# Optimization experiments

Measured on AMD Instinct MI355X. Metric: run time of the kernel, lower is better.

Reference implementation:

```python
import jax, jax.numpy as jnp
import numpy as np

N_NODES = 100000
N_EDGES = 1600000
N_GRAPHS = 512
HIDDEN = 128
N_LAYERS = 3


def setup_inputs() -> dict:
    key = jax.random.key(0)
    ks = jax.random.split(key, 16)
    X = jax.random.normal(ks[0], (N_NODES, HIDDEN), dtype=jnp.float32)
    edge_index = jax.random.randint(ks[1], (2, N_EDGES), 0, N_NODES, dtype=jnp.int64)
    batch = jnp.sort(jax.random.randint(ks[2], (N_NODES,), 0, N_GRAPHS, dtype=jnp.int64))
    s = 1.0 / np.sqrt(HIDDEN)
    mlp_w1 = jax.random.normal(ks[3], (N_LAYERS, HIDDEN, HIDDEN), dtype=jnp.float32) * s
    mlp_b1 = jnp.zeros((N_LAYERS, HIDDEN), dtype=jnp.float32)
    mlp_w2 = jax.random.normal(ks[4], (N_LAYERS, HIDDEN, HIDDEN), dtype=jnp.float32) * s
    mlp_b2 = jnp.zeros((N_LAYERS, HIDDEN), dtype=jnp.float32)
    cls_w1 = jax.random.normal(ks[5], (HIDDEN * N_LAYERS, HIDDEN), dtype=jnp.float32) / np.sqrt(HIDDEN * N_LAYERS)
    cls_b1 = jnp.zeros((HIDDEN,), dtype=jnp.float32)
    cls_w2 = jax.random.normal(ks[6], (HIDDEN, HIDDEN), dtype=jnp.float32) * s
    cls_b2 = jnp.zeros((HIDDEN,), dtype=jnp.float32)
    cls_w3 = jax.random.normal(ks[7], (HIDDEN, 1), dtype=jnp.float32) * s
    cls_b3 = jnp.zeros((1,), dtype=jnp.float32)
    return {"X": X, "edge_index": edge_index, "batch": batch,
            "mlp_w1": mlp_w1, "mlp_b1": mlp_b1, "mlp_w2": mlp_w2, "mlp_b2": mlp_b2,
            "cls_w1": cls_w1, "cls_b1": cls_b1, "cls_w2": cls_w2, "cls_b2": cls_b2,
            "cls_w3": cls_w3, "cls_b3": cls_b3}


def reference(X, edge_index, batch, mlp_w1, mlp_b1, mlp_w2, mlp_b2,
              cls_w1, cls_b1, cls_w2, cls_b2, cls_w3, cls_b3):
    src, dst = edge_index[0], edge_index[1]
    xs = []
    for l in range(N_LAYERS):
        # GIN aggregation: sum_{j in N(i)} x_j ; eps = 0 so add self feature
        agg = jax.ops.segment_sum(X[src], dst, num_segments=N_NODES)  # [N, H]
        z = X + agg
        # 2-layer MLP update
        h = jax.nn.relu(z @ mlp_w1[l] + mlp_b1[l])
        h = h @ mlp_w2[l] + mlp_b2[l]
        # dropout is identity in eval; then relu
        X = jax.nn.relu(h)
        # global sum pooling per graph
        xs.append(jax.ops.segment_sum(X, batch, num_segments=N_GRAPHS))  # [G, H]
    h = jnp.concatenate(xs, axis=-1)  # JK 'cat' -> [G, H*L]
    h = jax.nn.relu(h @ cls_w1 + cls_b1)
    h = jax.nn.relu(h @ cls_w2 + cls_b2)
    logits = h @ cls_w3 + cls_b3  # [G, 1]
    return logits
```

## Files before the change

kernel.cpp:

```cpp
#include <hip/hip_runtime.h>
#include <hip/hip_fp16.h>
#include <cstddef>
#include <cstdint>

#define N_NODES   100000
#define N_EDGES   1600000
#define N_GRAPHS  512
#define HIDDEN    128
#define N_LAYERS  3

#define N_WIN        400
#define WIN_NODES    (N_NODES / N_WIN)
#define PLACE_BLOCKS 128
#define PCHUNK       (N_EDGES / PLACE_BLOCKS)

#define F2H_BLOCKS   ((N_NODES * HIDDEN / 8) / 256)
#define WCONV_BLOCKS (N_LAYERS * 2 * 16)
#define GB_BLOCKS    2
#define PREPC_BLOCKS (PLACE_BLOCKS + F2H_BLOCKS + WCONV_BLOCKS + GB_BLOCKS)

typedef _Float16 half8  __attribute__((ext_vector_type(8)));
typedef _Float16 half4v __attribute__((ext_vector_type(4)));
typedef _Float16 half2v __attribute__((ext_vector_type(2)));
typedef float    float8 __attribute__((ext_vector_type(8)));
typedef float    floatx4 __attribute__((ext_vector_type(4)));
typedef float    floatx2 __attribute__((ext_vector_type(2)));

__global__ __launch_bounds__(256) void prep_count_kernel(const float* __restrict__ X,
                                                         unsigned char* __restrict__ outq,
                                                         const float* __restrict__ w1,
                                                         const float* __restrict__ w2,
                                                         __half* __restrict__ wt1,
                                                         __half* __restrict__ wt2,
                                                         const int* __restrict__ batch,
                                                         int* __restrict__ gstart,
                                                         const int* __restrict__ dst,
                                                         int* __restrict__ counts) {
    __shared__ float tile[32][33];
    __shared__ int   cs[N_WIN];
    const int b = blockIdx.x;
    if (b < PLACE_BLOCKS) {
        for (int i = threadIdx.x; i < N_WIN; i += 256) cs[i] = 0;
        __syncthreads();
        const int4* d4 = (const int4*)(dst + b * PCHUNK);
        for (int i = threadIdx.x; i < PCHUNK / 4; i += 256) {
            int4 d = d4[i];
            atomicAdd(&cs[d.x / WIN_NODES], 1);
            atomicAdd(&cs[d.y / WIN_NODES], 1);
            atomicAdd(&cs[d.z / WIN_NODES], 1);
            atomicAdd(&cs[d.w / WIN_NODES], 1);
        }
        __syncthreads();
        for (int i = threadIdx.x; i < N_WIN; i += 256)
            counts[i * PLACE_BLOCKS + b] = cs[i];
    } else if (b < PLACE_BLOCKS + F2H_BLOCKS) {
        int t = (b - PLACE_BLOCKS) * 256 + threadIdx.x;
        const float4* in4 = (const float4*)X;
        float4 a = in4[t * 2 + 0];
        float4 c = in4[t * 2 + 1];
        unsigned r0 = 0, r1 = 0;
        r0 = __builtin_amdgcn_cvt_pk_fp8_f32(a.x, a.y, r0, false);
        r0 = __builtin_amdgcn_cvt_pk_fp8_f32(a.z, a.w, r0, true);
        r1 = __builtin_amdgcn_cvt_pk_fp8_f32(c.x, c.y, r1, false);
        r1 = __builtin_amdgcn_cvt_pk_fp8_f32(c.z, c.w, r1, true);
        ((uint2*)outq)[t] = make_uint2(r0, r1);
    } else if (b < PLACE_BLOCKS + F2H_BLOCKS + WCONV_BLOCKS) {
        const int bb = b - PLACE_BLOCKS - F2H_BLOCKS;
        const int mat = bb & 1;
        const int tt = (bb >> 1) & 15;
        const int l  = bb >> 5;
        const int ti = (tt >> 2) * 32, tj = (tt & 3) * 32;
        const float* W = (mat ? w2 : w1) + (size_t)l * HIDDEN * HIDDEN;
        __half* WT = (mat ? wt2 : wt1) + (size_t)l * HIDDEN * HIDDEN;
        const int r = threadIdx.x >> 5;
        const int c = threadIdx.x & 31;
#pragma unroll
        for (int rr = 0; rr < 4; ++rr)
            tile[r + 8 * rr][c] = W[(size_t)(ti + r + 8 * rr) * HIDDEN + tj + c];
        __syncthreads();
#pragma unroll
        for (int rr = 0; rr < 4; ++rr)
            WT[(size_t)(tj + r + 8 * rr) * HIDDEN + ti + c] =
                __float2half(tile[c][r + 8 * rr]);
    } else {
        const int g = (b - PLACE_BLOCKS - F2H_BLOCKS - WCONV_BLOCKS) * 256 + threadIdx.x;
        if (g < N_GRAPHS) {
            int lo = 0, hi = N_NODES;
            while (lo < hi) {
                int mid = (lo + hi) >> 1;
                if (batch[mid] < g) lo = mid + 1; else hi = mid;
            }
            gstart[g] = lo;
        }
        if (g == 0) gstart[N_GRAPHS] = N_NODES;
    }
}

__global__ __launch_bounds__(512) void win_place_kernel(const int* __restrict__ src,
                                                        const int* __restrict__ dst,
                                                        const int* __restrict__ counts,
                                                        int* __restrict__ colsum,
                                                        int2* __restrict__ wedge) {
    __shared__ int ws[512];
    __shared__ int off[N_WIN];
    const int t = threadIdx.x;
    const int b = blockIdx.x;

    int total = 0, part = 0;
    if (t < N_WIN) {
        const int* col = counts + t * PLACE_BLOCKS;
#pragma unroll 4
        for (int bb = 0; bb < PLACE_BLOCKS; ++bb) {
            int v = col[bb];
            total += v;
            if (bb < b) part += v;
        }
        if (b == 0) colsum[t] = total;
    }
    ws[t] = (t < N_WIN) ? total : 0;
    __syncthreads();
#pragma unroll
    for (int o = 1; o < 512; o <<= 1) {
        int u = (t >= o) ? ws[t - o] : 0;
        __syncthreads();
        ws[t] += u;
        __syncthreads();
    }
    if (t < N_WIN) off[t] = part + ((t == 0) ? 0 : ws[t - 1]);
    __syncthreads();
    const int4* d4 = (const int4*)(dst + b * PCHUNK);
    const int4* s4 = (const int4*)(src + b * PCHUNK);
    for (int i = t; i < PCHUNK / 4; i += 512) {
        int4 d = d4[i];
        int4 s = s4[i];
        int p0 = atomicAdd(&off[d.x / WIN_NODES], 1); wedge[p0] = make_int2(d.x, s.x);
        int p1 = atomicAdd(&off[d.y / WIN_NODES], 1); wedge[p1] = make_int2(d.y, s.y);
        int p2 = atomicAdd(&off[d.z / WIN_NODES], 1); wedge[p2] = make_int2(d.z, s.z);
        int p3 = atomicAdd(&off[d.w / WIN_NODES], 1); wedge[p3] = make_int2(d.w, s.w);
    }
}

__global__ __launch_bounds__(512) void win_csr_kernel(const int2* __restrict__ wedge,
                                                      const int* __restrict__ colsum,
                                                      int* __restrict__ row_ptr,
                                                      int* __restrict__ csr_src) {
    __shared__ int ws[512];
    __shared__ int cnt[WIN_NODES];
    __shared__ int bb[2];
    const int w = blockIdx.x, n0 = w * WIN_NODES, t = threadIdx.x;
    ws[t] = (t < N_WIN) ? colsum[t] : 0;
    __syncthreads();
#pragma unroll
    for (int o = 1; o < 512; o <<= 1) {
        int u = (t >= o) ? ws[t - o] : 0;
        __syncthreads();
        ws[t] += u;
        __syncthreads();
    }
    if (t == 0) { bb[0] = (w > 0) ? ws[w - 1] : 0; bb[1] = ws[w]; }
    if (w == N_WIN - 1 && t == 0) row_ptr[N_NODES] = ws[N_WIN - 1];
    for (int i = t; i < WIN_NODES; i += 512) cnt[i] = 0;
    __syncthreads();
    const int b0 = bb[0], b1 = bb[1];
    for (int e = b0 + t; e < b1; e += 512)
        atomicAdd(&cnt[wedge[e].x - n0], 1);
    __syncthreads();
    ws[t] = (t < WIN_NODES) ? cnt[t] : 0;
    __syncthreads();
#pragma unroll
    for (int o = 1; o < 512; o <<= 1) {
        int u = (t >= o) ? ws[t - o] : 0;
        __syncthreads();
        ws[t] += u;
        __syncthreads();
    }
    const int excl = (t == 0) ? 0 : ws[t - 1];
    if (t < WIN_NODES) {
        row_ptr[n0 + t] = b0 + excl;
        cnt[t] = b0 + excl;
    }
    __syncthreads();
    for (int e = b0 + t; e < b1; e += 512) {
        int2 ed = wedge[e];
        int p = atomicAdd(&cnt[ed.x - n0], 1);
        csr_src[p] = ed.y;
    }
}

__device__ __forceinline__ void acc_fp8x16(floatx2* acc, uint4 v) {
    acc[0] += __builtin_amdgcn_cvt_pk_f32_fp8(v.x, false);
    acc[1] += __builtin_amdgcn_cvt_pk_f32_fp8(v.x, true);
    acc[2] += __builtin_amdgcn_cvt_pk_f32_fp8(v.y, false);
    acc[3] += __builtin_amdgcn_cvt_pk_f32_fp8(v.y, true);
    acc[4] += __builtin_amdgcn_cvt_pk_f32_fp8(v.z, false);
    acc[5] += __builtin_amdgcn_cvt_pk_f32_fp8(v.z, true);
    acc[6] += __builtin_amdgcn_cvt_pk_f32_fp8(v.w, false);
    acc[7] += __builtin_amdgcn_cvt_pk_f32_fp8(v.w, true);
}

__device__ __forceinline__ void gather_body(int wave, int lane,
                                            const unsigned char* __restrict__ Xq,
                                            __half* __restrict__ Zh,
                                            const int* __restrict__ row_ptr,
                                            const int* __restrict__ csr_src) {
    const int grp = lane >> 3;
    const int m   = lane & 7;
    const uint4* Q = (const uint4*)Xq;

    floatx2 acc[8];
#pragma unroll
    for (int j = 0; j < 8; ++j) acc[j] = floatx2{0.f, 0.f};

    if (grp == 0) {
        uint4 v = Q[(size_t)wave * 8 + m];
        acc_fp8x16(acc, v);
    }

    int k = row_ptr[wave];
    const int end = row_ptr[wave + 1];

    for (; k + 16 <= end; k += 16) {
        int n0 = csr_src[k + grp];
        int n1 = csr_src[k + 8 + grp];
        uint4 v0 = Q[(size_t)n0 * 8 + m];
        uint4 v1 = Q[(size_t)n1 * 8 + m];
        acc_fp8x16(acc, v0);
        acc_fp8x16(acc, v1);
    }
    if (k + 8 <= end) {
        int n0 = csr_src[k + grp];
        uint4 v0 = Q[(size_t)n0 * 8 + m];
        acc_fp8x16(acc, v0);
        k += 8;
    }
    int rem = end - k;
    if (grp < rem) {
        int n0 = csr_src[k + grp];
        uint4 v0 = Q[(size_t)n0 * 8 + m];
        acc_fp8x16(acc, v0);
    }

    half2v hh[8];
#pragma unroll
    for (int j = 0; j < 8; ++j) {
        hh[j][0] = (_Float16)acc[j][0];
        hh[j][1] = (_Float16)acc[j][1];
    }
#pragma unroll
    for (int j = 0; j < 8; ++j) {
        int b = __shfl_xor(__builtin_bit_cast(int, hh[j]), 8);
        hh[j] = hh[j] + __builtin_bit_cast(half2v, b);
    }
#pragma unroll
    for (int j = 0; j < 8; ++j) {
        int b = __shfl_xor(__builtin_bit_cast(int, hh[j]), 16);
        hh[j] = hh[j] + __builtin_bit_cast(half2v, b);
    }
#pragma unroll
    for (int j = 0; j < 8; ++j) {
        int b = __shfl_xor(__builtin_bit_cast(int, hh[j]), 32);
        hh[j] = hh[j] + __builtin_bit_cast(half2v, b);
    }

    if (grp == 0) {
        half8 o0, o1;
#pragma unroll
        for (int j = 0; j < 4; ++j) {
            o0[2 * j] = hh[j][0]; o0[2 * j + 1] = hh[j][1];
        }
#pragma unroll
        for (int j = 0; j < 4; ++j) {
            o1[2 * j] = hh[4 + j][0]; o1[2 * j + 1] = hh[4 + j][1];
        }
        ((half8*)(Zh + (size_t)wave * HIDDEN + 16 * m))[0] = o0;
        ((half8*)(Zh + (size_t)wave * HIDDEN + 16 * m))[1] = o1;
    }
}

__global__ void gather_kernel(const unsigned char* __restrict__ Xq,
                              __half* __restrict__ Zh,
                              const int* __restrict__ row_ptr,
                              const int* __restrict__ csr_src) {
    int wave = (blockIdx.x * blockDim.x + threadIdx.x) >> 6;
    if (wave >= N_NODES) return;
    gather_body(wave, threadIdx.x & 63, Xq, Zh, row_ptr, csr_src);
}

__device__ __forceinline__ void gpool_body(int g,
                                           const __half* __restrict__ Hpool,
                                           const int* __restrict__ gstart,
                                           float* __restrict__ pooled, int layer) {
    __shared__ float red[16][16][8];
    const int f8 = threadIdx.x & 15;
    const int qt = threadIdx.x >> 4;
    const int s = gstart[g], e = gstart[g + 1];

    float acc[8];
#pragma unroll
    for (int j = 0; j < 8; ++j) acc[j] = 0.f;

    for (int n = s + qt; n < e; n += 16) {
        half8 v = ((const half8*)(Hpool + (size_t)n * HIDDEN))[f8];
#pragma unroll
        for (int j = 0; j < 8; ++j) acc[j] += (float)v[j];
    }
#pragma unroll
    for (int j = 0; j < 8; ++j) red[qt][f8][j] = acc[j];
    __syncthreads();

    if (threadIdx.x < 128) {
        const int c = threadIdx.x;
        float sum = 0.f;
#pragma unroll
        for (int p = 0; p < 16; ++p) sum += red[p][c >> 3][c & 7];
        pooled[(size_t)g * (HIDDEN * N_LAYERS) + layer * HIDDEN + c] = sum;
    }
}

#define POOL_BLKS N_GRAPHS
__global__ __launch_bounds__(256) void gather_pool_kernel(const unsigned char* __restrict__ Xq,
                                                          const __half* __restrict__ Hpool,
                                                          __half* __restrict__ Zh,
                                                          const int* __restrict__ row_ptr,
                                                          const int* __restrict__ csr_src,
                                                          const int* __restrict__ gstart,
                                                          float* __restrict__ pooled,
                                                          int prev_layer) {
    if (blockIdx.x < POOL_BLKS) {
        gpool_body(blockIdx.x, Hpool, gstart, pooled, prev_layer);
        return;
    }
    int wave = ((blockIdx.x - POOL_BLKS) * 256 + threadIdx.x) >> 6;
    if (wave >= N_NODES) return;
    gather_body(wave, threadIdx.x & 63, Xq, Zh, row_ptr, csr_src);
}

__global__ __launch_bounds__(256) void gpool_cls_kernel(const __half* __restrict__ Xh,
                                                        const int* __restrict__ gstart,
                                                        const float* __restrict__ pooled,
                                                        const float* __restrict__ w1,
                                                        const float* __restrict__ b1,
                                                        const float* __restrict__ w2,
                                                        const float* __restrict__ b2,
                                                        const float* __restrict__ w3,
                                                        const float* __restrict__ b3,
                                                        float* __restrict__ out) {
    __shared__ float red[16][16][8];
    __shared__ float hin[HIDDEN * N_LAYERS];
    __shared__ float h1v[HIDDEN];
    __shared__ float redc[HIDDEN];
    const int g   = blockIdx.x;
    const int tid = threadIdx.x;
    const int f8  = tid & 15;
    const int qt  = tid >> 4;
    const int s = gstart[g], e = gstart[g + 1];

    for (int i = tid; i < 2 * HIDDEN; i += 256)
        hin[i] = pooled[(size_t)g * (HIDDEN * N_LAYERS) + i];

    float acc[8];
#pragma unroll
    for (int j = 0; j < 8; ++j) acc[j] = 0.f;
    for (int n = s + qt; n < e; n += 16) {
        half8 v = ((const half8*)(Xh + (size_t)n * HIDDEN))[f8];
#pragma unroll
        for (int j = 0; j < 8; ++j) acc[j] += (float)v[j];
    }
#pragma unroll
    for (int j = 0; j < 8; ++j) red[qt][f8][j] = acc[j];
    __syncthreads();
    if (tid < 128) {
        float sum = 0.f;
#pragma unroll
        for (int p = 0; p < 16; ++p) sum += red[p][tid >> 3][tid & 7];
        hin[2 * HIDDEN + tid] = sum;
    }
    __syncthreads();

    if (tid < 128) {
        float sacc = 0.f;
        for (int k = 0; k < HIDDEN * N_LAYERS; ++k)
            sacc += hin[k] * w1[(size_t)k * HIDDEN + tid];
        h1v[tid] = fmaxf(sacc + b1[tid], 0.f);
    }
    __syncthreads();
    if (tid < 128) {
        float s2 = 0.f;
        for (int k = 0; k < HIDDEN; ++k) s2 += h1v[k] * w2[(size_t)k * HIDDEN + tid];
        s2 = fmaxf(s2 + b2[tid], 0.f);
        redc[tid] = s2 * w3[tid];
    }
    __syncthreads();
    for (int off = 64; off > 0; off >>= 1) {
        if (tid < off) redc[tid] += redc[tid + off];
        __syncthreads();
    }
    if (tid == 0) out[g] = redc[0] + b3[0];
}

#define MMF_BLOCKS 512
__global__ __launch_bounds__(512, 4) void mlp_ws_kernel(const __half* __restrict__ A,
                                                        const __half* __restrict__ Wt1,
                                                        const __half* __restrict__ Wt2,
                                                        const float* __restrict__ b1,
                                                        const float* __restrict__ b2,
                                                        __half* __restrict__ C16,
                                                        unsigned char* __restrict__ Q8) {
    __shared__ _Float16 hs[2][16][128];

    const int tid  = threadIdx.x;
    const int wv   = tid >> 6;
    const int lane = tid & 63;
    const int m    = lane & 15;
    const int q    = lane >> 4;
    const int NTILES = N_NODES / 16;

    half8 wf1[4], wf2[4];
    float bl1[4], bl2[4];
    {
        const half8* W1row = (const half8*)(Wt1 + (size_t)(wv * 16 + m) * HIDDEN);
        const half8* W2row = (const half8*)(Wt2 + (size_t)(wv * 16 + m) * HIDDEN);
#pragma unroll
        for (int c = 0; c < 4; ++c) { wf1[c] = W1row[c * 4 + q]; wf2[c] = W2row[c * 4 + q]; }
#pragma unroll
        for (int r = 0; r < 4; ++r) {
            bl1[r] = b1[wv * 16 + q * 4 + r];
            bl2[r] = b2[wv * 16 + q * 4 + r];
        }
    }

    _Float16* hwr0 = &hs[0][m][(((2 * wv + (q >> 1)) ^ m) << 3) + ((q & 1) << 2)];
    _Float16* hwr1 = &hs[1][m][(((2 * wv + (q >> 1)) ^ m) << 3) + ((q & 1) << 2)];
    const _Float16* hrd0 = &hs[0][m][0];
    const _Float16* hrd1 = &hs[1][m][0];

    int t = blockIdx.x;
    half8 c0, c1, c2, c3, p0, p1, p2, p3;
    {
        const half8* Ar = (const half8*)(A + (size_t)(t * 16 + m) * HIDDEN);
        c0 = Ar[q]; c1 = Ar[4 + q]; c2 = Ar[8 + q]; c3 = Ar[12 + q];
    }
    if (t + MMF_BLOCKS < NTILES) {
        const half8* Ar = (const half8*)(A + (size_t)((t + MMF_BLOCKS) * 16 + m) * HIDDEN);
        p0 = Ar[q]; p1 = Ar[4 + q]; p2 = Ar[8 + q]; p3 = Ar[12 + q];
    }

    int buf = 0;
    while (true) {
        const int t2 = t + 2 * MMF_BLOCKS;
        half8 f0, f1, f2, f3;
        if (t2 < NTILES) {
            const half8* Ar = (const half8*)(A + (size_t)(t2 * 16 + m) * HIDDEN);
            f0 = Ar[q]; f1 = Ar[4 + q]; f2 = Ar[8 + q]; f3 = Ar[12 + q];
        }

        {
            floatx4 acc = {0.f, 0.f, 0.f, 0.f};
            acc = __builtin_amdgcn_mfma_f32_16x16x32_f16(wf1[0], c0, acc, 0, 0, 0);
            acc = __builtin_amdgcn_mfma_f32_16x16x32_f16(wf1[1], c1, acc, 0, 0, 0);
            acc = __builtin_amdgcn_mfma_f32_16x16x32_f16(wf1[2], c2, acc, 0, 0, 0);
            acc = __builtin_amdgcn_mfma_f32_16x16x32_f16(wf1[3], c3, acc, 0, 0, 0);
            half4v o;
#pragma unroll
            for (int r = 0; r < 4; ++r) o[r] = (_Float16)fmaxf(acc[r] + bl1[r], 0.f);
            *(half4v*)(buf ? hwr1 : hwr0) = o;
        }
        __builtin_amdgcn_sched_barrier(0);
        asm volatile("s_waitcnt lgkmcnt(0)" ::: "memory");
        __builtin_amdgcn_s_barrier();
        __builtin_amdgcn_sched_barrier(0);

        {
            const _Float16* hr = buf ? hrd1 : hrd0;
            half8 h0 = *(const half8*)(hr + (((0 + q) ^ m) << 3));
            half8 h1 = *(const half8*)(hr + (((4 + q) ^ m) << 3));
            half8 h2 = *(const half8*)(hr + (((8 + q) ^ m) << 3));
            half8 h3 = *(const half8*)(hr + (((12 + q) ^ m) << 3));
            floatx4 acc = {0.f, 0.f, 0.f, 0.f};
            acc = __builtin_amdgcn_mfma_f32_16x16x32_f16(wf2[0], h0, acc, 0, 0, 0);
            acc = __builtin_amdgcn_mfma_f32_16x16x32_f16(wf2[1], h1, acc, 0, 0, 0);
            acc = __builtin_amdgcn_mfma_f32_16x16x32_f16(wf2[2], h2, acc, 0, 0, 0);
            acc = __builtin_amdgcn_mfma_f32_16x16x32_f16(wf2[3], h3, acc, 0, 0, 0);
            float v0 = fmaxf(acc[0] + bl2[0], 0.f);
            float v1 = fmaxf(acc[1] + bl2[1], 0.f);
            float v2 = fmaxf(acc[2] + bl2[2], 0.f);
            float v3 = fmaxf(acc[3] + bl2[3], 0.f);
            const size_t base = (size_t)(t * 16 + m) * HIDDEN + wv * 16 + q * 4;
            half4v o;
            o[0] = (_Float16)v0; o[1] = (_Float16)v1;
            o[2] = (_Float16)v2; o[3] = (_Float16)v3;
            *(half4v*)(C16 + base) = o;
            if (Q8) {
                unsigned r0 = 0;
                r0 = __builtin_amdgcn_cvt_pk_fp8_f32(v0, v1, r0, false);
                r0 = __builtin_amdgcn_cvt_pk_fp8_f32(v2, v3, r0, true);
                *(unsigned*)(Q8 + base) = r0;
            }
        }

        if (t + MMF_BLOCKS >= NTILES) break;
        t += MMF_BLOCKS;
        c0 = p0; c1 = p1; c2 = p2; c3 = p3;
        p0 = f0; p1 = f1; p2 = f2; p3 = f3;
        buf ^= 1;
    }
}

extern "C" void kernel_launch(void* const* d_in, const int* in_sizes, int n_in,
                              void* d_out, int out_size, void* d_ws, size_t ws_size,
                              hipStream_t stream) {
    const float* X     = (const float*)d_in[0];
    const int*   ei    = (const int*)d_in[1];
    const int*   batch = (const int*)d_in[2];
    const float* w1all = (const float*)d_in[3];
    const float* b1all = (const float*)d_in[4];
    const float* w2all = (const float*)d_in[5];
    const float* b2all = (const float*)d_in[6];
    const float* cw1   = (const float*)d_in[7];
    const float* cb1   = (const float*)d_in[8];
    const float* cw2   = (const float*)d_in[9];
    const float* cb2   = (const float*)d_in[10];
    const float* cw3   = (const float*)d_in[11];
    const float* cb3   = (const float*)d_in[12];
    float* out = (float*)d_out;

    const int* src = ei;
    const int* dst = ei + N_EDGES;

    char* p = (char*)d_ws;
    auto alloc2 = [&](size_t bytes) {
        char* r = p;
        p += (bytes + 255) & ~(size_t)255;
        return r;
    };
    __half* hA      = (__half*)alloc2((size_t)N_NODES * HIDDEN * sizeof(__half));
    __half* hB      = (__half*)alloc2((size_t)N_NODES * HIDDEN * sizeof(__half));
    __half* zh      = (__half*)alloc2((size_t)N_NODES * HIDDEN * sizeof(__half));
    unsigned char* qbuf = (unsigned char*)alloc2((size_t)N_NODES * HIDDEN);
    __half* wt1     = (__half*)alloc2((size_t)N_LAYERS * HIDDEN * HIDDEN * sizeof(__half));
    __half* wt2     = (__half*)alloc2((size_t)N_LAYERS * HIDDEN * HIDDEN * sizeof(__half));
    int2*   wedge   = (int2*)alloc2((size_t)N_EDGES * sizeof(int2));
    int*    csr     = (int*)alloc2((size_t)N_EDGES * sizeof(int));
    int*    rowp    = (int*)alloc2((size_t)(N_NODES + 1) * sizeof(int));
    int*    counts  = (int*)alloc2((size_t)PLACE_BLOCKS * N_WIN * sizeof(int));
    int*    colsum  = (int*)alloc2((size_t)N_WIN * sizeof(int));
    int*    gstart  = (int*)alloc2((size_t)(N_GRAPHS + 1) * sizeof(int));
    float*  pooled  = (float*)alloc2((size_t)N_GRAPHS * HIDDEN * N_LAYERS * sizeof(float));

    prep_count_kernel<<<PREPC_BLOCKS, 256, 0, stream>>>(X, qbuf, w1all, w2all,
                                                        wt1, wt2, batch, gstart,
                                                        dst, counts);
    win_place_kernel<<<PLACE_BLOCKS, 512, 0, stream>>>(src, dst, counts, colsum, wedge);
    win_csr_kernel<<<N_WIN, 512, 0, stream>>>(wedge, colsum, rowp, csr);

    const int gat_grid = (N_NODES + 3) / 4;

    __half* hcur = nullptr;
    for (int l = 0; l < N_LAYERS; ++l) {
        __half* hnext = (l & 1) ? hA : hB;
        const bool emit = (l < N_LAYERS - 1);
        if (l == 0) {
            gather_kernel<<<gat_grid, 256, 0, stream>>>(qbuf, zh, rowp, csr);
        } else {
            gather_pool_kernel<<<gat_grid + POOL_BLKS, 256, 0, stream>>>(
                qbuf, hcur, zh, rowp, csr, gstart, pooled, l - 1);
        }
        mlp_ws_kernel<<<MMF_BLOCKS, 512, 0, stream>>>(zh,
                                                      wt1 + (size_t)l * HIDDEN * HIDDEN,
                                                      wt2 + (size_t)l * HIDDEN * HIDDEN,
                                                      b1all + (size_t)l * HIDDEN,
                                                      b2all + (size_t)l * HIDDEN,
                                                      hnext,
                                                      emit ? qbuf : (unsigned char*)nullptr);
        hcur = hnext;
    }

    gpool_cls_kernel<<<N_GRAPHS, 256, 0, stream>>>(hcur, gstart, pooled,
                                                   cw1, cb1, cw2, cb2, cw3, cb3, out);
}
```

Measured before the change: 426.9 us.

## Fuse neighbor gather into MLP kernel via LDS-staged tiles

Merges the per-node fp8 neighbor aggregation and the two-layer MFMA MLP into one persistent kernel. Each wave gathers two node rows into a swizzled LDS tile, which then feeds the MFMA directly. This removes the fp16 Z buffer write and read and one launch per layer. The fp8 feature buffer is now ping-ponged, since the kernel reads the previous features while writing new ones. The cost is that the gather latency is no longer hidden by the old register prefetch pipeline, and each tile now has an extra barrier.

```diff
diff --git a/kernel.cpp b/kernel.cpp
--- a/kernel.cpp
+++ b/kernel.cpp
@@ -22,7 +22,6 @@
 typedef _Float16 half8  __attribute__((ext_vector_type(8)));
 typedef _Float16 half4v __attribute__((ext_vector_type(4)));
 typedef _Float16 half2v __attribute__((ext_vector_type(2)));
-typedef float    float8 __attribute__((ext_vector_type(8)));
 typedef float    floatx4 __attribute__((ext_vector_type(4)));
 typedef float    floatx2 __attribute__((ext_vector_type(2)));
 
@@ -198,13 +197,13 @@
     acc[7] += __builtin_amdgcn_cvt_pk_f32_fp8(v.w, true);
 }
 
-__device__ __forceinline__ void gather_body(int wave, int lane,
-                                            const unsigned char* __restrict__ Xq,
-                                            __half* __restrict__ Zh,
-                                            const int* __restrict__ row_ptr,
-                                            const int* __restrict__ csr_src) {
+__device__ __forceinline__ void gather_node_lds(int node, int lane,
+                                                const unsigned char* __restrict__ Xq,
+                                                const int* __restrict__ row_ptr,
+                                                const int* __restrict__ csr_src,
+                                                _Float16* __restrict__ ztrow, int row) {
     const int grp = lane >> 3;
-    const int m   = lane & 7;
+    const int gm  = lane & 7;
     const uint4* Q = (const uint4*)Xq;
 
     floatx2 acc[8];
@@ -212,31 +211,31 @@
     for (int j = 0; j < 8; ++j) acc[j] = floatx2{0.f, 0.f};
 
     if (grp == 0) {
-        uint4 v = Q[(size_t)wave * 8 + m];
+        uint4 v = Q[(size_t)node * 8 + gm];
         acc_fp8x16(acc, v);
     }
 
-    int k = row_ptr[wave];
-    const int end = row_ptr[wave + 1];
+    int k = row_ptr[node];
+    const int end = row_ptr[node + 1];
 
     for (; k + 16 <= end; k += 16) {
         int n0 = csr_src[k + grp];
         int n1 = csr_src[k + 8 + grp];
-        uint4 v0 = Q[(size_t)n0 * 8 + m];
-        uint4 v1 = Q[(size_t)n1 * 8 + m];
+        uint4 v0 = Q[(size_t)n0 * 8 + gm];
+        uint4 v1 = Q[(size_t)n1 * 8 + gm];
         acc_fp8x16(acc, v0);
         acc_fp8x16(acc, v1);
     }
     if (k + 8 <= end) {
         int n0 = csr_src[k + grp];
-        uint4 v0 = Q[(size_t)n0 * 8 + m];
+        uint4 v0 = Q[(size_t)n0 * 8 + gm];
         acc_fp8x16(acc, v0);
         k += 8;
     }
     int rem = end - k;
     if (grp < rem) {
         int n0 = csr_src[k + grp];
-        uint4 v0 = Q[(size_t)n0 * 8 + m];
+        uint4 v0 = Q[(size_t)n0 * 8 + gm];
         acc_fp8x16(acc, v0);
     }
 
@@ -265,32 +264,19 @@
     if (grp == 0) {
         half8 o0, o1;
 #pragma unroll
-        for (int j = 0; j < 4; ++j) {
-            o0[2 * j] = hh[j][0]; o0[2 * j + 1] = hh[j][1];
-        }
-#pragma unroll
-        for (int j = 0; j < 4; ++j) {
-            o1[2 * j] = hh[4 + j][0]; o1[2 * j + 1] = hh[4 + j][1];
-        }
-        ((half8*)(Zh + (size_t)wave * HIDDEN + 16 * m))[0] = o0;
-        ((half8*)(Zh + (size_t)wave * HIDDEN + 16 * m))[1] = o1;
-    }
-}
-
-__global__ void gather_kernel(const unsigned char* __restrict__ Xq,
-                              __half* __restrict__ Zh,
-                              const int* __restrict__ row_ptr,
-                              const int* __restrict__ csr_src) {
-    int wave = (blockIdx.x * blockDim.x + threadIdx.x) >> 6;
-    if (wave >= N_NODES) return;
-    gather_body(wave, threadIdx.x & 63, Xq, Zh, row_ptr, csr_src);
-}
-
-__device__ __forceinline__ void gpool_body(int g,
-                                           const __half* __restrict__ Hpool,
-                                           const int* __restrict__ gstart,
-                                           float* __restrict__ pooled, int layer) {
-    __shared__ float red[16][16][8];
+        for (int j = 0; j < 4; ++j) { o0[2 * j] = hh[j][0]; o0[2 * j + 1] = hh[j][1]; }
+#pragma unroll
+        for (int j = 0; j < 4; ++j) { o1[2 * j] = hh[4 + j][0]; o1[2 * j + 1] = hh[4 + j][1]; }
+        *(half8*)&ztrow[((2 * gm) ^ row) << 3]     = o0;
+        *(half8*)&ztrow[((2 * gm + 1) ^ row) << 3] = o1;
+    }
+}
+
+__device__ __forceinline__ void gpool_body512(int g,
+                                              const __half* __restrict__ H,
+                                              const int* __restrict__ gstart,
+                                              float* __restrict__ pooled, int layer) {
+    __shared__ float red[32][16][8];
     const int f8 = threadIdx.x & 15;
     const int qt = threadIdx.x >> 4;
     const int s = gstart[g], e = gstart[g + 1];
@@ -298,115 +284,48 @@
     float acc[8];
 #pragma unroll
     for (int j = 0; j < 8; ++j) acc[j] = 0.f;
-
-    for (int n = s + qt; n < e; n += 16) {
-        half8 v = ((const half8*)(Hpool + (size_t)n * HIDDEN))[f8];
+    for (int n = s + qt; n < e; n += 32) {
+        half8 v = ((const half8*)(H + (size_t)n * HIDDEN))[f8];
 #pragma unroll
         for (int j = 0; j < 8; ++j) acc[j] += (float)v[j];
     }
 #pragma unroll
     for (int j = 0; j < 8; ++j) red[qt][f8][j] = acc[j];
     __syncthreads();
-
     if (threadIdx.x < 128) {
         const int c = threadIdx.x;
         float sum = 0.f;
 #pragma unroll
-        for (int p = 0; p < 16; ++p) sum += red[p][c >> 3][c & 7];
+        for (int p = 0; p < 32; ++p) sum += red[p][c >> 3][c & 7];
         pooled[(size_t)g * (HIDDEN * N_LAYERS) + layer * HIDDEN + c] = sum;
     }
 }
 
 #define POOL_BLKS N_GRAPHS
-__global__ __launch_bounds__(256) void gather_pool_kernel(const unsigned char* __restrict__ Xq,
-                                                          const __half* __restrict__ Hpool,
-                                                          __half* __restrict__ Zh,
-                                                          const int* __restrict__ row_ptr,
-                                                          const int* __restrict__ csr_src,
-                                                          const int* __restrict__ gstart,
-                                                          float* __restrict__ pooled,
-                                                          int prev_layer) {
-    if (blockIdx.x < POOL_BLKS) {
-        gpool_body(blockIdx.x, Hpool, gstart, pooled, prev_layer);
+#define GM_BLOCKS 1024
+__global__ __launch_bounds__(512, 4) void gather_mlp_kernel(
+        const unsigned char* __restrict__ Xq,
+        const __half* __restrict__ Hpool,
+        const int* __restrict__ row_ptr,
+        const int* __restrict__ csr_src,
+        const __half* __restrict__ Wt1,
+        const __half* __restrict__ Wt2,
+        const float* __restrict__ b1,
+        const float* __restrict__ b2,
+        const int* __restrict__ gstart,
+        float* __restrict__ pooled,
+        int prev_layer,
+        __half* __restrict__ C16,
+        unsigned char* __restrict__ Q8) {
+    __shared__ _Float16 zt[2][16][128];
+    __shared__ _Float16 hs[2][16][128];
+
+    const bool has_pool = (prev_layer >= 0);
+    if (has_pool && blockIdx.x < POOL_BLKS) {
+        gpool_body512(blockIdx.x, Hpool, gstart, pooled, prev_layer);
         return;
     }
-    int wave = ((blockIdx.x - POOL_BLKS) * 256 + threadIdx.x) >> 6;
-    if (wave >= N_NODES) return;
-    gather_body(wave, threadIdx.x & 63, Xq, Zh, row_ptr, csr_src);
-}
-
-__global__ __launch_bounds__(256) void gpool_cls_kernel(const __half* __restrict__ Xh,
-                                                        const int* __restrict__ gstart,
-                                                        const float* __restrict__ pooled,
-                                                        const float* __restrict__ w1,
-                                                        const float* __restrict__ b1,
-                                                        const float* __restrict__ w2,
-                                                        const float* __restrict__ b2,
-                                                        const float* __restrict__ w3,
-                                                        const float* __restrict__ b3,
-                                                        float* __restrict__ out) {
-    __shared__ float red[16][16][8];
-    __shared__ float hin[HIDDEN * N_LAYERS];
-    __shared__ float h1v[HIDDEN];
-    __shared__ float redc[HIDDEN];
-    const int g   = blockIdx.x;
-    const int tid = threadIdx.x;
-    const int f8  = tid & 15;
-    const int qt  = tid >> 4;
-    const int s = gstart[g], e = gstart[g + 1];
-
-    for (int i = tid; i < 2 * HIDDEN; i += 256)
-        hin[i] = pooled[(size_t)g * (HIDDEN * N_LAYERS) + i];
-
-    float acc[8];
-#pragma unroll
-    for (int j = 0; j < 8; ++j) acc[j] = 0.f;
-    for (int n = s + qt; n < e; n += 16) {
-        half8 v = ((const half8*)(Xh + (size_t)n * HIDDEN))[f8];
-#pragma unroll
-        for (int j = 0; j < 8; ++j) acc[j] += (float)v[j];
-    }
-#pragma unroll
-    for (int j = 0; j < 8; ++j) red[qt][f8][j] = acc[j];
-    __syncthreads();
-    if (tid < 128) {
-        float sum = 0.f;
-#pragma unroll
-        for (int p = 0; p < 16; ++p) sum += red[p][tid >> 3][tid & 7];
-        hin[2 * HIDDEN + tid] = sum;
-    }
-    __syncthreads();
-
-    if (tid < 128) {
-        float sacc = 0.f;
-        for (int k = 0; k < HIDDEN * N_LAYERS; ++k)
-            sacc += hin[k] * w1[(size_t)k * HIDDEN + tid];
-        h1v[tid] = fmaxf(sacc + b1[tid], 0.f);
-    }
-    __syncthreads();
-    if (tid < 128) {
-        float s2 = 0.f;
-        for (int k = 0; k < HIDDEN; ++k) s2 += h1v[k] * w2[(size_t)k * HIDDEN + tid];
-        s2 = fmaxf(s2 + b2[tid], 0.f);
-        redc[tid] = s2 * w3[tid];
-    }
-    __syncthreads();
-    for (int off = 64; off > 0; off >>= 1) {
-        if (tid < off) redc[tid] += redc[tid + off];
-        __syncthreads();
-    }
-    if (tid == 0) out[g] = redc[0] + b3[0];
-}
-
-#define MMF_BLOCKS 512
-__global__ __launch_bounds__(512, 4) void mlp_ws_kernel(const __half* __restrict__ A,
-                                                        const __half* __restrict__ Wt1,
-                                                        const __half* __restrict__ Wt2,
-                                                        const float* __restrict__ b1,
-                                                        const float* __restrict__ b2,
-                                                        __half* __restrict__ C16,
-                                                        unsigned char* __restrict__ Q8) {
-    __shared__ _Float16 hs[2][16][128];
+    const int gb = blockIdx.x - (has_pool ? POOL_BLKS : 0);
 
     const int tid  = threadIdx.x;
     const int wv   = tid >> 6;
@@ -429,41 +348,13 @@
         }
     }
 
-    _Float16* hwr0 = &hs[0][m][(((2 * wv + (q >> 1)) ^ m) << 3) + ((q & 1) << 2)];
-    _Float16* hwr1 = &hs[1][m][(((2 * wv + (q >> 1)) ^ m) << 3) + ((q & 1) << 2)];
-    const _Float16* hrd0 = &hs[0][m][0];
-    const _Float16* hrd1 = &hs[1][m][0];
-
-    int t = blockIdx.x;
-    half8 c0, c1, c2, c3, p0, p1, p2, p3;
-    {
-        const half8* Ar = (const half8*)(A + (size_t)(t * 16 + m) * HIDDEN);
-        c0 = Ar[q]; c1 = Ar[4 + q]; c2 = Ar[8 + q]; c3 = Ar[12 + q];
-    }
-    if (t + MMF_BLOCKS < NTILES) {
-        const half8* Ar = (const half8*)(A + (size_t)((t + MMF_BLOCKS) * 16 + m) * HIDDEN);
-        p0 = Ar[q]; p1 = Ar[4 + q]; p2 = Ar[8 + q]; p3 = Ar[12 + q];
-    }
-
     int buf = 0;
-    while (true) {
-        const int t2 = t + 2 * MMF_BLOCKS;
-        half8 f0, f1, f2, f3;
-        if (t2 < NTILES) {
-            const half8* Ar = (const half8*)(A + (size_t)(t2 * 16 + m) * HIDDEN);
-            f0 = Ar[q]; f1 = Ar[4 + q]; f2 = Ar[8 + q]; f3 = Ar[12 + q];
-        }
-
-        {
-            floatx4 acc = {0.f, 0.f, 0.f, 0.f};
-            acc = __builtin_amdgcn_mfma_f32_16x16x32_f16(wf1[0], c0, acc, 0, 0, 0);
-            acc = __builtin_amdgcn_mfma_f32_16x16x32_f16(wf1[1], c1, acc, 0, 0, 0);
-            acc = __builtin_amdgcn_mfma_f32_16x16x32_f16(wf1[2], c2, acc, 0, 0, 0);
-            acc = __builtin_amdgcn_mfma_f32_16x16x32_f16(wf1[3], c3, acc, 0, 0, 0);
-            half4v o;
-#pragma unroll
-            for (int r = 0; r < 4; ++r) o[r] = (_Float16)fmaxf(acc[r] + bl1[r], 0.f);
-            *(half4v*)(buf ? hwr1 : hwr0) = o;
+    for (int t = gb; t < NTILES; t += GM_BLOCKS) {
+#pragma unroll
+        for (int s = 0; s < 2; ++s) {
+            const int row = 2 * wv + s;
+            gather_node_lds(t * 16 + row, lane, Xq, row_ptr, csr_src,
+                            &zt[buf][row][0], row);
         }
         __builtin_amdgcn_sched_barrier(0);
         asm volatile("s_waitcnt lgkmcnt(0)" ::: "memory");
@@ -471,7 +362,28 @@
         __builtin_amdgcn_sched_barrier(0);
 
         {
-            const _Float16* hr = buf ? hrd1 : hrd0;
+            const _Float16* ar = &zt[buf][m][0];
+            half8 a0 = *(const half8*)(ar + (((0 + q) ^ m) << 3));
+            half8 a1 = *(const half8*)(ar + (((4 + q) ^ m) << 3));
+            half8 a2 = *(const half8*)(ar + (((8 + q) ^ m) << 3));
+            half8 a3 = *(const half8*)(ar + (((12 + q) ^ m) << 3));
+            floatx4 acc = {0.f, 0.f, 0.f, 0.f};
+            acc = __builtin_amdgcn_mfma_f32_16x16x32_f16(wf1[0], a0, acc, 0, 0, 0);
+            acc = __builtin_amdgcn_mfma_f32_16x16x32_f16(wf1[1], a1, acc, 0, 0, 0);
+            acc = __builtin_amdgcn_mfma_f32_16x16x32_f16(wf1[2], a2, acc, 0, 0, 0);
+            acc = __builtin_amdgcn_mfma_f32_16x16x32_f16(wf1[3], a3, acc, 0, 0, 0);
+            half4v o;
+#pragma unroll
+            for (int r = 0; r < 4; ++r) o[r] = (_Float16)fmaxf(acc[r] + bl1[r], 0.f);
+            *(half4v*)&hs[buf][m][(((2 * wv + (q >> 1)) ^ m) << 3) + ((q & 1) << 2)] = o;
+        }
+        __builtin_amdgcn_sched_barrier(0);
+        asm volatile("s_waitcnt lgkmcnt(0)" ::: "memory");
+        __builtin_amdgcn_s_barrier();
+        __builtin_amdgcn_sched_barrier(0);
+
+        {
+            const _Float16* hr = &hs[buf][m][0];
             half8 h0 = *(const half8*)(hr + (((0 + q) ^ m) << 3));
             half8 h1 = *(const half8*)(hr + (((4 + q) ^ m) << 3));
             half8 h2 = *(const half8*)(hr + (((8 + q) ^ m) << 3));
@@ -497,13 +409,71 @@
                 *(unsigned*)(Q8 + base) = r0;
             }
         }
-
-        if (t + MMF_BLOCKS >= NTILES) break;
-        t += MMF_BLOCKS;
-        c0 = p0; c1 = p1; c2 = p2; c3 = p3;
-        p0 = f0; p1 = f1; p2 = f2; p3 = f3;
         buf ^= 1;
     }
+}
+
+__global__ __launch_bounds__(256) void gpool_cls_kernel(const __half* __restrict__ Xh,
+                                                        const int* __restrict__ gstart,
+                                                        const float* __restrict__ pooled,
+                                                        const float* __restrict__ w1,
+                                                        const float* __restrict__ b1,
+                                                        const float* __restrict__ w2,
+                                                        const float* __restrict__ b2,
+                                                        const float* __restrict__ w3,
+                                                        const float* __restrict__ b3,
+                                                        float* __restrict__ out) {
+    __shared__ float red[16][16][8];
+    __shared__ float hin[HIDDEN * N_LAYERS];
+    __shared__ float h1v[HIDDEN];
+    __shared__ float redc[HIDDEN];
+    const int g   = blockIdx.x;
+    const int tid = threadIdx.x;
+    const int f8  = tid & 15;
+    const int qt  = tid >> 4;
+    const int s = gstart[g], e = gstart[g + 1];
+
+    for (int i = tid; i < 2 * HIDDEN; i += 256)
+        hin[i] = pooled[(size_t)g * (HIDDEN * N_LAYERS) + i];
+
+    float acc[8];
+#pragma unroll
+    for (int j = 0; j < 8; ++j) acc[j] = 0.f;
+    for (int n = s + qt; n < e; n += 16) {
+        half8 v = ((const half8*)(Xh + (size_t)n * HIDDEN))[f8];
+#pragma unroll
+        for (int j = 0; j < 8; ++j) acc[j] += (float)v[j];
+    }
+#pragma unroll
+    for (int j = 0; j < 8; ++j) red[qt][f8][j] = acc[j];
+    __syncthreads();
+    if (tid < 128) {
+        float sum = 0.f;
+#pragma unroll
+        for (int p = 0; p < 16; ++p) sum += red[p][tid >> 3][tid & 7];
+        hin[2 * HIDDEN + tid] = sum;
+    }
+    __syncthreads();
+
+    if (tid < 128) {
+        float sacc = 0.f;
+        for (int k = 0; k < HIDDEN * N_LAYERS; ++k)
+            sacc += hin[k] * w1[(size_t)k * HIDDEN + tid];
+        h1v[tid] = fmaxf(sacc + b1[tid], 0.f);
+    }
+    __syncthreads();
+    if (tid < 128) {
+        float s2 = 0.f;
+        for (int k = 0; k < HIDDEN; ++k) s2 += h1v[k] * w2[(size_t)k * HIDDEN + tid];
+        s2 = fmaxf(s2 + b2[tid], 0.f);
+        redc[tid] = s2 * w3[tid];
+    }
+    __syncthreads();
+    for (int off = 64; off > 0; off >>= 1) {
+        if (tid < off) redc[tid] += redc[tid + off];
+        __syncthreads();
+    }
+    if (tid == 0) out[g] = redc[0] + b3[0];
 }
 
 extern "C" void kernel_launch(void* const* d_in, const int* in_sizes, int n_in,
@@ -535,8 +505,8 @@
     };
     __half* hA      = (__half*)alloc2((size_t)N_NODES * HIDDEN * sizeof(__half));
     __half* hB      = (__half*)alloc2((size_t)N_NODES * HIDDEN * sizeof(__half));
-    __half* zh      = (__half*)alloc2((size_t)N_NODES * HIDDEN * sizeof(__half));
-    unsigned char* qbuf = (unsigned char*)alloc2((size_t)N_NODES * HIDDEN);
+    unsigned char* qA = (unsigned char*)alloc2((size_t)N_NODES * HIDDEN);
+    unsigned char* qB = (unsigned char*)alloc2((size_t)N_NODES * HIDDEN);
     __half* wt1     = (__half*)alloc2((size_t)N_LAYERS * HIDDEN * HIDDEN * sizeof(__half));
     __half* wt2     = (__half*)alloc2((size_t)N_LAYERS * HIDDEN * HIDDEN * sizeof(__half));
     int2*   wedge   = (int2*)alloc2((size_t)N_EDGES * sizeof(int2));
@@ -547,32 +517,29 @@
     int*    gstart  = (int*)alloc2((size_t)(N_GRAPHS + 1) * sizeof(int));
     float*  pooled  = (float*)alloc2((size_t)N_GRAPHS * HIDDEN * N_LAYERS * sizeof(float));
 
-    prep_count_kernel<<<PREPC_BLOCKS, 256, 0, stream>>>(X, qbuf, w1all, w2all,
+    prep_count_kernel<<<PREPC_BLOCKS, 256, 0, stream>>>(X, qA, w1all, w2all,
                                                         wt1, wt2, batch, gstart,
                                                         dst, counts);
     win_place_kernel<<<PLACE_BLOCKS, 512, 0, stream>>>(src, dst, counts, colsum, wedge);
     win_csr_kernel<<<N_WIN, 512, 0, stream>>>(wedge, colsum, rowp, csr);
 
-    const int gat_grid = (N_NODES + 3) / 4;
-
+    unsigned char* qin  = qA;
+    unsigned char* qout = qB;
     __half* hcur = nullptr;
     for (int l = 0; l < N_LAYERS; ++l) {
         __half* hnext = (l & 1) ? hA : hB;
         const bool emit = (l < N_LAYERS - 1);
-        if (l == 0) {
-            gather_kernel<<<gat_grid, 256, 0, stream>>>(qbuf, zh, rowp, csr);
-        } else {
-            gather_pool_kernel<<<gat_grid + POOL_BLKS, 256, 0, stream>>>(
-                qbuf, hcur, zh, rowp, csr, gstart, pooled, l - 1);
-        }
-        mlp_ws_kernel<<<MMF_BLOCKS, 512, 0, stream>>>(zh,
-                                                      wt1 + (size_t)l * HIDDEN * HIDDEN,
-                                                      wt2 + (size_t)l * HIDDEN * HIDDEN,
-                                                      b1all + (size_t)l * HIDDEN,
-                                                      b2all + (size_t)l * HIDDEN,
-                                                      hnext,
-                                                      emit ? qbuf : (unsigned char*)nullptr);
+        const int grid = GM_BLOCKS + ((l > 0) ? POOL_BLKS : 0);
+        gather_mlp_kernel<<<grid, 512, 0, stream>>>(
+            qin, hcur, rowp, csr,
+            wt1 + (size_t)l * HIDDEN * HIDDEN,
+            wt2 + (size_t)l * HIDDEN * HIDDEN,
+            b1all + (size_t)l * HIDDEN,
+            b2all + (size_t)l * HIDDEN,
+            gstart, pooled, l - 1,
+            hnext, emit ? qout : (unsigned char*)nullptr);
         hcur = hnext;
+        unsigned char* tmp = qin; qin = qout; qout = tmp;
     }
 
     gpool_cls_kernel<<<N_GRAPHS, 256, 0, stream>>>(hcur, gstart, pooled,
```

Result: slower. 520.9 us (+22.0%).
